# Kernel optimization log

Measured on AMD Instinct MI355X. Metric: run time of the kernel, lower is better.

## Reference

```python
import jax, jax.numpy as jnp
import numpy as np

B, N, D, K = 2, 8192, 512, 16


def setup_inputs() -> dict:
    key = jax.random.key(0)
    k1, k2, k3, k4 = jax.random.split(key, 4)
    x = jax.random.normal(k1, (B, N, D), dtype=jnp.float32)
    xyz = jax.random.normal(k2, (B, N, 3), dtype=jnp.float32)
    # nn.Linear(d_model, 3*d_model): weight [3D, D], bias [3D]
    W_qkv = jax.random.normal(k3, (3 * D, D), dtype=jnp.float32) * 0.02
    b_qkv = jnp.zeros((3 * D,), dtype=jnp.float32)
    # nn.Linear(d_model, d_model)
    W_fc = jax.random.normal(k4, (D, D), dtype=jnp.float32) * 0.02
    b_fc = jnp.zeros((D,), dtype=jnp.float32)
    return {"x": x, "xyz": xyz, "W_qkv": W_qkv, "b_qkv": b_qkv, "W_fc": W_fc, "b_fc": b_fc}


def _knn_idx(xyz):
    # squared-distance KNN (same ordering as cdist): |a|^2 + |b|^2 - 2 a.b
    sq = jnp.sum(xyz * xyz, axis=-1)                      # [B, N]
    d2 = sq[:, :, None] + sq[:, None, :] - 2.0 * jnp.einsum('bnc,bmc->bnm', xyz, xyz)
    return jax.lax.top_k(-d2, K)[1]                       # [B, N, K] smallest distances


def reference(x, xyz, W_qkv, b_qkv, W_fc, b_fc):
    knn_idx = _knn_idx(xyz)                               # no-grad in original
    qkv = jnp.einsum('bnd,ed->bne', x, W_qkv) + b_qkv     # [B, N, 3D]
    qkv = qkv.reshape(B, N, 3, D)
    q, k, v = qkv[:, :, 0], qkv[:, :, 1], qkv[:, :, 2]    # [B, N, D]
    gather = jax.vmap(lambda arr, idx: arr[idx])          # per-batch neighbor gather
    k_neigh = gather(k, knn_idx)                          # [B, N, K, D]
    v_neigh = gather(v, knn_idx)                          # [B, N, K, D]
    # faithful to einsum('bnd,bnsk->bns', q, k_neigh): sums d and feature dims independently
    attn = (q.sum(-1)[:, :, None] * k_neigh.sum(-1)) / jnp.sqrt(jnp.float32(D))  # [B, N, K]
    attn = jax.nn.softmax(attn, axis=2)[..., None]        # [B, N, K, 1]
    x_out = (attn * v_neigh).sum(axis=2)                  # [B, N, D]
    return jnp.einsum('bnd,ed->bne', x_out, W_fc) + b_fc + x
```

## Files before the change

### kernel.cpp

```cpp
#include <hip/hip_runtime.h>

typedef _Float16 half_t;
typedef _Float16 half8 __attribute__((ext_vector_type(8)));
typedef _Float16 half4v __attribute__((ext_vector_type(4)));
typedef float f32x4 __attribute__((ext_vector_type(4)));
typedef float f32x2 __attribute__((ext_vector_type(2)));

#define NB 2
#define NN 8192
#define ND 512
#define NKNN 16
#define BN (NB*NN)

#define OFF_XH   0ull
#define OFF_VH   (OFF_XH  + (size_t)BN*ND*2)
#define OFF_XOH  (OFF_VH  + (size_t)BN*ND*2)
#define OFF_WVH  (OFF_XOH + (size_t)BN*ND*2)
#define OFF_WFCH (OFF_WVH + (size_t)ND*ND*2)
#define OFF_XW   (OFF_WFCH+ (size_t)ND*ND*2)
#define OFF_XW2  (OFF_XW  + (size_t)BN*16)
#define OFF_IDX  (OFF_XW2 + (size_t)BN*16)
#define OFF_WQC  (OFF_IDX + (size_t)BN*NKNN*4)
#define OFF_WKC  (OFF_WQC + 2048)
#define OFF_QKB  (OFF_WKC + 2048)
#define OFF_QS   (OFF_QKB + 256)
#define OFF_KS   (OFF_QS  + (size_t)BN*4)

__device__ __forceinline__ void gload16(const void* g, void* l) {
  __builtin_amdgcn_global_load_lds((const __attribute__((address_space(1))) void*)g,
                                   (__attribute__((address_space(3))) void*)l, 16, 0, 0);
}

__global__ __launch_bounds__(256) void ksetup(const float* __restrict__ wqkv,
                                              const float* __restrict__ bqkv,
                                              const float* __restrict__ wfc,
                                              const float* __restrict__ xyz,
                                              float* __restrict__ wq, float* __restrict__ wk,
                                              float* __restrict__ qkb,
                                              half_t* __restrict__ wvh, half_t* __restrict__ wfch,
                                              float4* __restrict__ xw, float4* __restrict__ xw2) {
  const int blk = blockIdx.x;
  const int t = threadIdx.x;
  if (blk < 16) {
    int h = blk >> 3, g = blk & 7;
    int dl = t & 63, s = t >> 6;
    const float* Wb = wqkv + (size_t)h * 512 * 512;
    int d = g * 64 + dl;
    float acc = 0.f;
    for (int e = s * 128; e < s * 128 + 128; ++e) acc += Wb[(size_t)e * 512 + d];
    __shared__ float red[4][64];
    red[s][dl] = acc;
    __syncthreads();
    if (s == 0) (h ? wk : wq)[d] = red[0][dl] + red[1][dl] + red[2][dl] + red[3][dl];
  } else if (blk == 16) {
    __shared__ float r0[256], r1[256];
    r0[t] = bqkv[t] + bqkv[t + 256];
    r1[t] = bqkv[512 + t] + bqkv[768 + t];
    __syncthreads();
    for (int s = 128; s; s >>= 1) {
      if (t < s) { r0[t] += r0[t + s]; r1[t] += r1[t + s]; }
      __syncthreads();
    }
    if (t == 0) { qkb[0] = r0[0]; qkb[1] = r1[0]; }
  } else if (blk < 273) {
    int i = (blk - 17) * 256 + t;
    float4 a = ((const float4*)(wqkv + 1024 * 512))[i];
    half4v ha; ha[0]=(half_t)a.x; ha[1]=(half_t)a.y; ha[2]=(half_t)a.z; ha[3]=(half_t)a.w;
    *(half4v*)(wvh + (size_t)i * 4) = ha;
    float4 c = ((const float4*)wfc)[i];
    half4v hc; hc[0]=(half_t)c.x; hc[1]=(half_t)c.y; hc[2]=(half_t)c.z; hc[3]=(half_t)c.w;
    *(half4v*)(wfch + (size_t)i * 4) = hc;
  } else {
    int p = (blk - 273) * 256 + t;
    int b = p >> 12;
    int pl = p & 4095;
    int i0 = b * NN + pl * 2;
    const float* s = xyz + (size_t)i0 * 3;
    float x0 = s[0], y0 = s[1], z0 = s[2];
    float x1 = s[3], y1 = s[4], z1 = s[5];
    float sq0 = __fadd_rn(__fadd_rn(__fmul_rn(x0, x0), __fmul_rn(y0, y0)), __fmul_rn(z0, z0));
    float sq1 = __fadd_rn(__fadd_rn(__fmul_rn(x1, x1), __fmul_rn(y1, y1)), __fmul_rn(z1, z1));
    xw[i0]     = make_float4(x0, y0, z0, sq0);
    xw[i0 + 1] = make_float4(x1, y1, z1, sq1);
    xw2[(size_t)b * NN + pl]        = make_float4(x0, x1, y0, y1);
    xw2[(size_t)b * NN + NN/2 + pl] = make_float4(z0, z1, sq0, sq1);
  }
}

__global__ __launch_bounds__(256) void kxh(const float* __restrict__ x,
                                           const float* __restrict__ wq,
                                           const float* __restrict__ wk,
                                           const float* __restrict__ qkb,
                                           half_t* __restrict__ xh,
                                           float* __restrict__ qs,
                                           float* __restrict__ ks) {
  int wid = blockIdx.x * 4 + (threadIdx.x >> 6);
  int l = threadIdx.x & 63;
  size_t base = (size_t)wid * ND + l * 8;
  float4 a0 = *(const float4*)(x + base);
  float4 a1 = *(const float4*)(x + base + 4);
  half8 h;
  h[0]=(half_t)a0.x; h[1]=(half_t)a0.y; h[2]=(half_t)a0.z; h[3]=(half_t)a0.w;
  h[4]=(half_t)a1.x; h[5]=(half_t)a1.y; h[6]=(half_t)a1.z; h[7]=(half_t)a1.w;
  *(half8*)(xh + base) = h;
  float4 q0 = ((const float4*)(wq + l * 8))[0], q1 = ((const float4*)(wq + l * 8))[1];
  float4 k0 = ((const float4*)(wk + l * 8))[0], k1 = ((const float4*)(wk + l * 8))[1];
  float dq = a0.x*q0.x + a0.y*q0.y + a0.z*q0.z + a0.w*q0.w
           + a1.x*q1.x + a1.y*q1.y + a1.z*q1.z + a1.w*q1.w;
  float dk = a0.x*k0.x + a0.y*k0.y + a0.z*k0.z + a0.w*k0.w
           + a1.x*k1.x + a1.y*k1.y + a1.z*k1.z + a1.w*k1.w;
  #pragma unroll
  for (int o = 32; o; o >>= 1) { dq += __shfl_xor(dq, o); dk += __shfl_xor(dk, o); }
  if (l == 0) { qs[wid] = dq + qkb[0]; ks[wid] = dk + qkb[1]; }
}

#define QPW 4
#define KTILE 512
__global__ __launch_bounds__(256, 4) void kknn(const float4* __restrict__ xw,
                                               const float4* __restrict__ xw2,
                                               int* __restrict__ idxo) {
  __shared__ __align__(16) float4 ldsA[2][KTILE];
  __shared__ __align__(16) float4 ldsB[2][KTILE];
  const int tid = threadIdx.x;
  const int l = tid & 63;
  const int w = tid >> 6;
  const int b = blockIdx.x >> 9;
  const int qbase = (blockIdx.x & 511) * (4 * QPW) + w * QPW;
  const float4* xb  = xw  + (size_t)b * NN;
  const float4* xa2 = xw2 + (size_t)b * NN;
  const float4* xb2 = xa2 + NN / 2;

#define STAGE(t, bi) do {                                                        \
    int ts_ = (t) * KTILE;                                                       \
    gload16(xa2 + ts_ +       w * 64 + l, (void*)&ldsA[bi][      w * 64]);       \
    gload16(xa2 + ts_ + 256 + w * 64 + l, (void*)&ldsA[bi][256 + w * 64]);       \
    gload16(xb2 + ts_ +       w * 64 + l, (void*)&ldsB[bi][      w * 64]);       \
    gload16(xb2 + ts_ + 256 + w * 64 + l, (void*)&ldsB[bi][256 + w * 64]);       \
  } while (0)

  f32x2 qxx[QPW], qyy[QPW], qzz[QPW], qww[QPW];
  #pragma unroll
  for (int qi = 0; qi < QPW; ++qi) {
    float4 qp = xb[qbase + qi];
    qxx[qi] = (f32x2){qp.x, qp.x};
    qyy[qi] = (f32x2){qp.y, qp.y};
    qzz[qi] = (f32x2){qp.z, qp.z};
    qww[qi] = (f32x2){qp.w, qp.w};
  }
  const f32x2 m2 = (f32x2){-2.0f, -2.0f};

  f32x2 mind[QPW];
  #pragma unroll
  for (int qi = 0; qi < QPW; ++qi) mind[qi] = (f32x2){__builtin_inff(), __builtin_inff()};

  STAGE(0, 0);
  __syncthreads();
  for (int t = 0; t < 8; ++t) {
    if (t < 7) STAGE(t + 1, (t + 1) & 1);
    #pragma unroll
    for (int it = 0; it < 8; ++it) {
      int p = it * 64 + l;
      float4 A  = ldsA[t & 1][p];
      float4 Bv = ldsB[t & 1][p];
      f32x2 cx = (f32x2){A.x, A.y};
      f32x2 cy = (f32x2){A.z, A.w};
      f32x2 cz = (f32x2){Bv.x, Bv.y};
      f32x2 cw = (f32x2){Bv.z, Bv.w};
      #pragma unroll
      for (int qi = 0; qi < QPW; ++qi) {
        f32x2 dot = __builtin_elementwise_fma(qzz[qi], cz,
                      __builtin_elementwise_fma(qyy[qi], cy, qxx[qi] * cx));
        f32x2 s2 = qww[qi] + cw;
        f32x2 d2 = __builtin_elementwise_fma(m2, dot, s2);
        mind[qi] = __builtin_elementwise_min(mind[qi], d2);
      }
    }
    __syncthreads();
  }

  float wst[QPW];
  #pragma unroll
  for (int qi = 0; qi < QPW; ++qi) {
    float d = fminf(mind[qi][0], mind[qi][1]);
    #pragma unroll
    for (int k = 2; k <= 64; k <<= 1) {
      #pragma unroll
      for (int j = k >> 1; j > 0; j >>= 1) {
        float od = __shfl_xor(d, j);
        bool up = ((l & k) == 0);
        bool lower_lane = ((l & j) == 0);
        bool oless = od < d;
        bool take = (up == lower_lane) ? oless : !oless;
        if (take) d = od;
      }
    }
    wst[qi] = __shfl(d, 15);
  }

  float kd[QPW]; int ki[QPW];
  #pragma unroll
  for (int qi = 0; qi < QPW; ++qi) { kd[qi] = __builtin_inff(); ki[qi] = 0x7fffffff; }

  auto insert = [&](bool ok, float dv, int iv, int qi) {
    unsigned long long m = __ballot(ok);
    while (m) {
      int a = __builtin_ctzll(m);
      m &= m - 1;
      float dc = __shfl(dv, a);
      int ic = __shfl(iv, a);
      bool lower = (kd[qi] < dc) || (kd[qi] == dc && ki[qi] < ic);
      int r = __popcll(__ballot(lower) & 0xFFFFull);
      if (r < 16) {
        float pd = __shfl_up(kd[qi], 1, 16);
        int pi = __shfl_up(ki[qi], 1, 16);
        int pp = l & 15;
        if (pp == r)      { kd[qi] = dc; ki[qi] = ic; }
        else if (pp > r)  { kd[qi] = pd; ki[qi] = pi; }
        wst[qi] = fminf(wst[qi], __shfl(kd[qi], 15, 16));
      }
    }
  };

  __syncthreads();
  STAGE(0, 0);
  __syncthreads();
  for (int t = 0; t < 8; ++t) {
    if (t < 7) STAGE(t + 1, (t + 1) & 1);
    #pragma unroll 2
    for (int it = 0; it < 8; ++it) {
      int p = it * 64 + l;
      float4 A  = ldsA[t & 1][p];
      float4 Bv = ldsB[t & 1][p];
      f32x2 cx = (f32x2){A.x, A.y};
      f32x2 cy = (f32x2){A.z, A.w};
      f32x2 cz = (f32x2){Bv.x, Bv.y};
      f32x2 cw = (f32x2){Bv.z, Bv.w};
      int ci0 = (t * KTILE + p) * 2;
      #pragma unroll
      for (int qi = 0; qi < QPW; ++qi) {
        f32x2 dot = __builtin_elementwise_fma(qzz[qi], cz,
                      __builtin_elementwise_fma(qyy[qi], cy, qxx[qi] * cx));
        f32x2 s2 = qww[qi] + cw;
        f32x2 d2 = __builtin_elementwise_fma(m2, dot, s2);
        bool ok0 = d2[0] <= wst[qi];
        bool ok1 = d2[1] <= wst[qi];
        if (__ballot(ok0 || ok1)) {
          insert(ok0, d2[0], ci0, qi);
          insert(ok1, d2[1], ci0 + 1, qi);
        }
      }
    }
    __syncthreads();
  }

  if (l < 16) {
    #pragma unroll
    for (int qi = 0; qi < QPW; ++qi)
      idxo[((size_t)b * NN + qbase + qi) * NKNN + l] = ki[qi];
  }
#undef STAGE
}

template <int EPI>
__global__ __launch_bounds__(256) void kgemm(const half_t* __restrict__ A,
                                             const half_t* __restrict__ Bw,
                                             const float* __restrict__ bias,
                                             const float* __restrict__ resid,
                                             void* __restrict__ Cout) {
  __shared__ __align__(16) half_t As[128 * 64];
  __shared__ __align__(16) half_t Bs[128 * 64];
  const int tid = threadIdx.x;
  const int l = tid & 63;
  const int w = tid >> 6;
  const int wm = w >> 1, wn = w & 1;
  const int mt = blockIdx.x >> 2;
  const int nt = blockIdx.x & 3;
  const int lr = l & 15, lg = l >> 4;

  f32x4 acc[4][4];
  #pragma unroll
  for (int i = 0; i < 4; ++i)
    #pragma unroll
    for (int j = 0; j < 4; ++j) acc[i][j] = (f32x4){0.f, 0.f, 0.f, 0.f};

  for (int kt = 0; kt < 8; ++kt) {
    #pragma unroll
    for (int i = 0; i < 4; ++i) {
      int id = i * 256 + tid;
      int rr = id >> 3, cc = id & 7;
      gload16(A + (size_t)(mt * 128 + rr) * ND + kt * 64 + cc * 8,
              (void*)(As + (size_t)(i * 256 + w * 64) * 8));
      gload16(Bw + (size_t)(nt * 128 + rr) * ND + kt * 64 + cc * 8,
              (void*)(Bs + (size_t)(i * 256 + w * 64) * 8));
    }
    __syncthreads();
    #pragma unroll
    for (int kk = 0; kk < 2; ++kk) {
      half8 af[4], bf[4];
      #pragma unroll
      for (int mi = 0; mi < 4; ++mi)
        af[mi] = *(const half8*)(As + (wm * 64 + mi * 16 + lr) * 64 + kk * 32 + lg * 8);
      #pragma unroll
      for (int ni = 0; ni < 4; ++ni)
        bf[ni] = *(const half8*)(Bs + (wn * 64 + ni * 16 + lr) * 64 + kk * 32 + lg * 8);
      #pragma unroll
      for (int mi = 0; mi < 4; ++mi)
        #pragma unroll
        for (int ni = 0; ni < 4; ++ni)
          acc[mi][ni] = __builtin_amdgcn_mfma_f32_16x16x32_f16(af[mi], bf[ni], acc[mi][ni], 0, 0, 0);
    }
    __syncthreads();
  }

  #pragma unroll
  for (int mi = 0; mi < 4; ++mi) {
    #pragma unroll
    for (int ni = 0; ni < 4; ++ni) {
      int col = nt * 128 + wn * 64 + ni * 16 + lr;
      #pragma unroll
      for (int r4 = 0; r4 < 4; ++r4) {
        size_t row = (size_t)mt * 128 + wm * 64 + mi * 16 + lg * 4 + r4;
        float v = acc[mi][ni][r4] + bias[col];
        if (EPI == 0) ((half_t*)Cout)[row * ND + col] = (half_t)v;
        else          ((float*)Cout)[row * ND + col] = v + resid[row * ND + col];
      }
    }
  }
}

__global__ __launch_bounds__(256) void kattn(const int* __restrict__ idx,
                                             const float* __restrict__ qs,
                                             const float* __restrict__ ks,
                                             const half_t* __restrict__ vh,
                                             half_t* __restrict__ xoh) {
  int wid = blockIdx.x * 4 + (threadIdx.x >> 6);
  int l = threadIdx.x & 63;
  int b = wid >> 13;
  int j = l & 15;
  int nb = idx[(size_t)wid * NKNN + j];
  float ksv = ks[(size_t)b * NN + nb];
  float logit = __fdiv_rn(__fmul_rn(qs[wid], ksv), 22.627416997969522f);
  float mx = logit;
  #pragma unroll
  for (int o = 8; o; o >>= 1) mx = fmaxf(mx, __shfl_xor(mx, o, 16));
  float e = expf(logit - mx);
  float s = e;
  #pragma unroll
  for (int o = 8; o; o >>= 1) s += __shfl_xor(s, o, 16);
  float p = e / s;

  float acc[8] = {0.f, 0.f, 0.f, 0.f, 0.f, 0.f, 0.f, 0.f};
  #pragma unroll
  for (int t16 = 0; t16 < 16; ++t16) {
    float wj = __shfl(p, t16, 16);
    int ij = __shfl(nb, t16, 16);
    const half8 vv = *(const half8*)(vh + ((size_t)b * NN + ij) * ND + l * 8);
    #pragma unroll
    for (int u = 0; u < 8; ++u) acc[u] += wj * (float)vv[u];
  }
  half8 ho;
  #pragma unroll
  for (int u = 0; u < 8; ++u) ho[u] = (half_t)acc[u];
  *(half8*)(xoh + (size_t)wid * ND + l * 8) = ho;
}

extern "C" void kernel_launch(void* const* d_in, const int* in_sizes, int n_in,
                              void* d_out, int out_size, void* d_ws, size_t ws_size,
                              hipStream_t stream) {
  const float* x    = (const float*)d_in[0];
  const float* xyz  = (const float*)d_in[1];
  const float* wqkv = (const float*)d_in[2];
  const float* bqkv = (const float*)d_in[3];
  const float* wfc  = (const float*)d_in[4];
  const float* bfc  = (const float*)d_in[5];
  char* ws = (char*)d_ws;
  half_t* xh   = (half_t*)(ws + OFF_XH);
  half_t* vh   = (half_t*)(ws + OFF_VH);
  half_t* xoh  = (half_t*)(ws + OFF_XOH);
  half_t* wvh  = (half_t*)(ws + OFF_WVH);
  half_t* wfch = (half_t*)(ws + OFF_WFCH);
  float4* xw   = (float4*)(ws + OFF_XW);
  float4* xw2  = (float4*)(ws + OFF_XW2);
  int*    idx  = (int*)(ws + OFF_IDX);
  float*  wqc  = (float*)(ws + OFF_WQC);
  float*  wkc  = (float*)(ws + OFF_WKC);
  float*  qkb  = (float*)(ws + OFF_QKB);
  float*  qs   = (float*)(ws + OFF_QS);
  float*  ks   = (float*)(ws + OFF_KS);

  ksetup<<<dim3(305), dim3(256), 0, stream>>>(wqkv, bqkv, wfc, xyz,
                                              wqc, wkc, qkb, wvh, wfch, xw, xw2);
  kxh   <<<dim3(4096),dim3(256), 0, stream>>>(x, wqc, wkc, qkb, xh, qs, ks);
  kknn  <<<dim3(1024),dim3(256), 0, stream>>>(xw, xw2, idx);
  kgemm<0><<<dim3(512),dim3(256), 0, stream>>>(xh, wvh, bqkv + 1024, (const float*)nullptr, (void*)vh);
  kattn <<<dim3(4096),dim3(256), 0, stream>>>(idx, qs, ks, vh, xoh);
  kgemm<1><<<dim3(512),dim3(256), 0, stream>>>(xoh, wfch, bfc, x, d_out);
}
```

Before: 156.5 us.

## Split KNN candidate range across two blocks and merge partial top-16 lists

```diff
diff --git a/kernel.cpp b/kernel.cpp
--- a/kernel.cpp
+++ b/kernel.cpp
@@ -20,7 +20,9 @@
 #define OFF_XW   (OFF_WFCH+ (size_t)ND*ND*2)
 #define OFF_XW2  (OFF_XW  + (size_t)BN*16)
 #define OFF_IDX  (OFF_XW2 + (size_t)BN*16)
-#define OFF_WQC  (OFF_IDX + (size_t)BN*NKNN*4)
+#define OFF_DH   (OFF_IDX + (size_t)BN*NKNN*4)
+#define OFF_IH   (OFF_DH  + (size_t)BN*2*NKNN*4)
+#define OFF_WQC  (OFF_IH  + (size_t)BN*2*NKNN*4)
 #define OFF_WKC  (OFF_WQC + 2048)
 #define OFF_QKB  (OFF_WKC + 2048)
 #define OFF_QS   (OFF_QKB + 256)
@@ -114,21 +116,24 @@
   if (l == 0) { qs[wid] = dq + qkb[0]; ks[wid] = dk + qkb[1]; }
 }
 
-#define QPW 4
+#define QPW 8
 #define KTILE 512
 __global__ __launch_bounds__(256, 4) void kknn(const float4* __restrict__ xw,
                                                const float4* __restrict__ xw2,
-                                               int* __restrict__ idxo) {
+                                               float* __restrict__ dhalf,
+                                               int* __restrict__ ihalf) {
   __shared__ __align__(16) float4 ldsA[2][KTILE];
   __shared__ __align__(16) float4 ldsB[2][KTILE];
   const int tid = threadIdx.x;
   const int l = tid & 63;
   const int w = tid >> 6;
-  const int b = blockIdx.x >> 9;
-  const int qbase = (blockIdx.x & 511) * (4 * QPW) + w * QPW;
+  const int g = blockIdx.x >> 1;
+  const int h = blockIdx.x & 1;
+  const int b = g >> 8;
+  const int qbase = (g & 255) * 32 + w * QPW;
   const float4* xb  = xw  + (size_t)b * NN;
-  const float4* xa2 = xw2 + (size_t)b * NN;
-  const float4* xb2 = xa2 + NN / 2;
+  const float4* xa2 = xw2 + (size_t)b * NN + h * 2048;
+  const float4* xb2 = xw2 + (size_t)b * NN + NN / 2 + h * 2048;
 
 #define STAGE(t, bi) do {                                                        \
     int ts_ = (t) * KTILE;                                                       \
@@ -155,8 +160,8 @@
 
   STAGE(0, 0);
   __syncthreads();
-  for (int t = 0; t < 8; ++t) {
-    if (t < 7) STAGE(t + 1, (t + 1) & 1);
+  for (int t = 0; t < 4; ++t) {
+    if (t < 3) STAGE(t + 1, (t + 1) & 1);
     #pragma unroll
     for (int it = 0; it < 8; ++it) {
       int p = it * 64 + l;
@@ -224,8 +229,8 @@
   __syncthreads();
   STAGE(0, 0);
   __syncthreads();
-  for (int t = 0; t < 8; ++t) {
-    if (t < 7) STAGE(t + 1, (t + 1) & 1);
+  for (int t = 0; t < 4; ++t) {
+    if (t < 3) STAGE(t + 1, (t + 1) & 1);
     #pragma unroll 2
     for (int it = 0; it < 8; ++it) {
       int p = it * 64 + l;
@@ -235,7 +240,7 @@
       f32x2 cy = (f32x2){A.z, A.w};
       f32x2 cz = (f32x2){Bv.x, Bv.y};
       f32x2 cw = (f32x2){Bv.z, Bv.w};
-      int ci0 = (t * KTILE + p) * 2;
+      int ci0 = h * 4096 + (t * KTILE + p) * 2;
       #pragma unroll
       for (int qi = 0; qi < QPW; ++qi) {
         f32x2 dot = __builtin_elementwise_fma(qzz[qi], cz,
@@ -255,10 +260,36 @@
 
   if (l < 16) {
     #pragma unroll
-    for (int qi = 0; qi < QPW; ++qi)
-      idxo[((size_t)b * NN + qbase + qi) * NKNN + l] = ki[qi];
+    for (int qi = 0; qi < QPW; ++qi) {
+      size_t o = (((size_t)(b * NN + qbase + qi)) * 2 + h) * NKNN + l;
+      dhalf[o] = kd[qi];
+      ihalf[o] = ki[qi];
+    }
   }
 #undef STAGE
+}
+
+__global__ __launch_bounds__(256) void kmerge(const float* __restrict__ dhalf,
+                                              const int* __restrict__ ihalf,
+                                              int* __restrict__ idxo) {
+  const int l = threadIdx.x & 63;
+  const int wv = threadIdx.x >> 6;
+  const int q = blockIdx.x * 8 + wv * 2 + (l >> 5);
+  const int sub = l & 31;
+  const int pos = (sub < 16) ? sub : 31 - sub;
+  const int hh  = (sub < 16) ? 0 : 1;
+  size_t o = (((size_t)q) * 2 + hh) * NKNN + pos;
+  float d = dhalf[o];
+  int   i = ihalf[o];
+  #pragma unroll
+  for (int j = 16; j; j >>= 1) {
+    float od = __shfl_xor(d, j, 32);
+    int   oi = __shfl_xor(i, j, 32);
+    bool oless = (od < d) || (od == d && oi < i);
+    bool keepmin = ((sub & j) == 0);
+    if (keepmin == oless) { d = od; i = oi; }
+  }
+  if (sub < 16) idxo[(size_t)q * NKNN + sub] = i;
 }
 
 template <int EPI>
@@ -382,6 +413,8 @@
   float4* xw   = (float4*)(ws + OFF_XW);
   float4* xw2  = (float4*)(ws + OFF_XW2);
   int*    idx  = (int*)(ws + OFF_IDX);
+  float*  dh   = (float*)(ws + OFF_DH);
+  int*    ih   = (int*)(ws + OFF_IH);
   float*  wqc  = (float*)(ws + OFF_WQC);
   float*  wkc  = (float*)(ws + OFF_WKC);
   float*  qkb  = (float*)(ws + OFF_QKB);
@@ -391,7 +424,8 @@
   ksetup<<<dim3(305), dim3(256), 0, stream>>>(wqkv, bqkv, wfc, xyz,
                                               wqc, wkc, qkb, wvh, wfch, xw, xw2);
   kxh   <<<dim3(4096),dim3(256), 0, stream>>>(x, wqc, wkc, qkb, xh, qs, ks);
-  kknn  <<<dim3(1024),dim3(256), 0, stream>>>(xw, xw2, idx);
+  kknn  <<<dim3(1024),dim3(256), 0, stream>>>(xw, xw2, dh, ih);
+  kmerge<<<dim3(2048),dim3(256), 0, stream>>>(dh, ih, idx);
   kgemm<0><<<dim3(512),dim3(256), 0, stream>>>(xh, wvh, bqkv + 1024, (const float*)nullptr, (void*)vh);
   kattn <<<dim3(4096),dim3(256), 0, stream>>>(idx, qs, ks, vh, xoh);
   kgemm<1><<<dim3(512),dim3(256), 0, stream>>>(xoh, wfch, bfc, x, d_out);
```

Result: slower. 177.7 us (+13.6%).

## Replace serial KNN top-16 insertion with LDS candidate append and bitonic sort

Applied to the files above, without the earlier changes.

```diff
diff --git a/kernel.cpp b/kernel.cpp
--- a/kernel.cpp
+++ b/kernel.cpp
@@ -121,6 +121,8 @@
                                                int* __restrict__ idxo) {
   __shared__ __align__(16) float4 ldsA[2][KTILE];
   __shared__ __align__(16) float4 ldsB[2][KTILE];
+  __shared__ float qdl[16 * 64];
+  __shared__ int   qil[16 * 64];
   const int tid = threadIdx.x;
   const int l = tid & 63;
   const int w = tid >> 6;
@@ -149,6 +151,12 @@
   }
   const f32x2 m2 = (f32x2){-2.0f, -2.0f};
 
+  #pragma unroll
+  for (int qi = 0; qi < QPW; ++qi) {
+    qdl[(w * 4 + qi) * 64 + l] = __builtin_inff();
+    qil[(w * 4 + qi) * 64 + l] = 0x7fffffff;
+  }
+
   f32x2 mind[QPW];
   #pragma unroll
   for (int qi = 0; qi < QPW; ++qi) mind[qi] = (f32x2){__builtin_inff(), __builtin_inff()};
@@ -197,29 +205,10 @@
     wst[qi] = __shfl(d, 15);
   }
 
-  float kd[QPW]; int ki[QPW];
-  #pragma unroll
-  for (int qi = 0; qi < QPW; ++qi) { kd[qi] = __builtin_inff(); ki[qi] = 0x7fffffff; }
-
-  auto insert = [&](bool ok, float dv, int iv, int qi) {
-    unsigned long long m = __ballot(ok);
-    while (m) {
-      int a = __builtin_ctzll(m);
-      m &= m - 1;
-      float dc = __shfl(dv, a);
-      int ic = __shfl(iv, a);
-      bool lower = (kd[qi] < dc) || (kd[qi] == dc && ki[qi] < ic);
-      int r = __popcll(__ballot(lower) & 0xFFFFull);
-      if (r < 16) {
-        float pd = __shfl_up(kd[qi], 1, 16);
-        int pi = __shfl_up(ki[qi], 1, 16);
-        int pp = l & 15;
-        if (pp == r)      { kd[qi] = dc; ki[qi] = ic; }
-        else if (pp > r)  { kd[qi] = pd; ki[qi] = pi; }
-        wst[qi] = fminf(wst[qi], __shfl(kd[qi], 15, 16));
-      }
-    }
-  };
+  int qcnt[QPW];
+  #pragma unroll
+  for (int qi = 0; qi < QPW; ++qi) qcnt[qi] = 0;
+  const unsigned long long below = (l == 63) ? ~0ull >> 1 : (1ull << l) - 1;
 
   __syncthreads();
   STAGE(0, 0);
@@ -244,19 +233,47 @@
         f32x2 d2 = __builtin_elementwise_fma(m2, dot, s2);
         bool ok0 = d2[0] <= wst[qi];
         bool ok1 = d2[1] <= wst[qi];
-        if (__ballot(ok0 || ok1)) {
-          insert(ok0, d2[0], ci0, qi);
-          insert(ok1, d2[1], ci0 + 1, qi);
+        unsigned long long m0 = __ballot(ok0);
+        if (m0) {
+          int slot = qcnt[qi] + __popcll(m0 & below);
+          if (ok0 && slot < 64) {
+            qdl[(w * 4 + qi) * 64 + slot] = d2[0];
+            qil[(w * 4 + qi) * 64 + slot] = ci0;
+          }
+          qcnt[qi] += __popcll(m0);
+        }
+        unsigned long long m1 = __ballot(ok1);
+        if (m1) {
+          int slot = qcnt[qi] + __popcll(m1 & below);
+          if (ok1 && slot < 64) {
+            qdl[(w * 4 + qi) * 64 + slot] = d2[1];
+            qil[(w * 4 + qi) * 64 + slot] = ci0 + 1;
+          }
+          qcnt[qi] += __popcll(m1);
         }
       }
     }
     __syncthreads();
   }
 
-  if (l < 16) {
-    #pragma unroll
-    for (int qi = 0; qi < QPW; ++qi)
-      idxo[((size_t)b * NN + qbase + qi) * NKNN + l] = ki[qi];
+  #pragma unroll
+  for (int qi = 0; qi < QPW; ++qi) {
+    float d = qdl[(w * 4 + qi) * 64 + l];
+    int  ii = qil[(w * 4 + qi) * 64 + l];
+    #pragma unroll
+    for (int k = 2; k <= 64; k <<= 1) {
+      #pragma unroll
+      for (int j = k >> 1; j > 0; j >>= 1) {
+        float od = __shfl_xor(d, j);
+        int   oi = __shfl_xor(ii, j);
+        bool up = ((l & k) == 0);
+        bool lower_lane = ((l & j) == 0);
+        bool oless = (od < d) || (od == d && oi < ii);
+        bool take = (up == lower_lane) ? oless : !oless;
+        if (take) { d = od; ii = oi; }
+      }
+    }
+    if (l < 16) idxo[((size_t)b * NN + qbase + qi) * NKNN + l] = ii;
   }
 #undef STAGE
 }
```

Result: faster. 145.3 us (-7.1%).
